# Optimization experiments

Measured on AMD Instinct MI355X. Metric: run time of the kernel, lower is better.

## Reference

```python
import jax, jax.numpy as jnp
import numpy as np

OUTPUT_SIZES = [1, 3, 6, 8]  # SPP pyramid -> total KV length 110

def _bounds(n, out):
    # PyTorch AdaptiveMaxPool2d bin boundaries
    return [((i * n) // out, -((-(i + 1) * n) // out)) for i in range(out)]

def adaptive_max_pool2d(x, out):
    # x: [B, C, H, W] -> [B, C, out, out]
    B, C, H, W = x.shape
    rows = jnp.stack([x[:, :, s:e, :].max(axis=2) for s, e in _bounds(H, out)], axis=2)
    return jnp.stack([rows[:, :, :, s:e].max(axis=3) for s, e in _bounds(W, out)], axis=3)

def spp(x):
    # [B, C, H, W] -> [B, C, S] with S = sum(o*o) = 110
    B, C = x.shape[:2]
    return jnp.concatenate(
        [adaptive_max_pool2d(x, o).reshape(B, C, o * o) for o in OUTPUT_SIZES], axis=2)

def conv1x1(x, w):
    # 1x1 conv, no bias: w [O, C], x [B, C, H, W]
    return jnp.einsum('oc,bchw->bohw', w, x)

def setup_inputs() -> dict:
    key = jax.random.key(0)
    ks = jax.random.split(key, 6)
    B, C, H, W = 16, 512, 64, 64
    IC = C // 2
    x = jax.random.normal(ks[0], (B, C, H, W), jnp.float32)
    y = jax.random.normal(ks[1], (B, C, H, W), jnp.float32)
    sc = 1.0 / np.sqrt(C)
    w_phi = jax.random.normal(ks[2], (IC, C), jnp.float32) * sc
    w_theta = jax.random.normal(ks[3], (IC, C), jnp.float32) * sc
    w_g = jax.random.normal(ks[4], (IC, C), jnp.float32) * sc
    w_mask = jax.random.normal(ks[5], (C, IC), jnp.float32) * (1.0 / np.sqrt(IC))
    return {"x": x, "y": y, "w_phi": w_phi, "w_theta": w_theta,
            "w_g": w_g, "w_mask": w_mask}

def reference(x, y, w_phi, w_theta, w_g, w_mask):
    B, C, H, W = x.shape
    IC = w_phi.shape[0]
    N = H * W
    # Query: [B, N, IC]
    x_phi = conv1x1(x, w_phi).reshape(B, IC, N).transpose(0, 2, 1)
    # Keys/values from SPP-pooled y: [B, IC, S] / [B, S, IC]
    y_theta = spp(conv1x1(y, w_theta))
    y_g = spp(conv1x1(y, w_g)).transpose(0, 2, 1)
    # Attention with softmax over the QUERY axis (dim=1), as in the source
    attn = jax.nn.softmax(jnp.einsum('bnc,bcs->bns', x_phi, y_theta), axis=1)
    agg = jnp.einsum('bns,bsc->bnc', attn, y_g)          # [B, N, IC]
    agg = agg.transpose(0, 2, 1).reshape(B, IC, H, W)     # [B, IC, H, W]
    mask = conv1x1(agg, w_mask)                           # [B, C, H, W]
    return mask + x
```

## Files before the change

### kernel.cpp

```cpp
#include <hip/hip_runtime.h>

#define DI __device__ __forceinline__

typedef __attribute__((ext_vector_type(8))) __bf16 bf16x8;
typedef __attribute__((ext_vector_type(4))) float f32x4;

DI unsigned short f2bf(float x) {
  union { float f; unsigned u; } v; v.f = x;
  unsigned r = v.u + 0x7fffu + ((v.u >> 16) & 1u);
  return (unsigned short)(r >> 16);
}
DI float bf2f(unsigned short h) {
  union { unsigned u; float f; } v; v.u = ((unsigned)h) << 16;
  return v.f;
}
DI unsigned pack2(float a, float b) {
  return (unsigned)f2bf(a) | (((unsigned)f2bf(b)) << 16);
}

__global__ __launch_bounds__(256) void k1_conv_tg(
    const float* __restrict__ y, const float* __restrict__ w_theta,
    const float* __restrict__ w_g, unsigned short* __restrict__ tg)
{
  const int tid = threadIdx.x;
  const int nb = blockIdx.x * 128;
  const int mb = blockIdx.y * 128;
  const int b  = blockIdx.z;
  const int lane = tid & 63, wv = tid >> 6;
  const int wm = (wv & 1) * 64, wn = (wv >> 1) * 64;
  const int l15 = lane & 15, l4 = lane >> 4;

  __shared__ unsigned short Ah[128 * 40];
  __shared__ unsigned short Bt[128 * 40];

  f32x4 acc[4][4];
  #pragma unroll
  for (int i = 0; i < 4; ++i)
    #pragma unroll
    for (int j = 0; j < 4; ++j) acc[i][j] = f32x4{0.f, 0.f, 0.f, 0.f};

  for (int kb = 0; kb < 512; kb += 32) {
    #pragma unroll
    for (int j = 0; j < 4; ++j) {
      int flat = tid + 256 * j;
      int row = flat >> 3, c4 = (flat & 7) << 2;
      int og = mb + row;
      const float* wr = (og < 256) ? (w_theta + (size_t)og * 512)
                                   : (w_g + (size_t)(og - 256) * 512);
      float4 v = *(const float4*)(wr + kb + c4);
      uint2 u; u.x = pack2(v.x, v.y); u.y = pack2(v.z, v.w);
      *(uint2*)&Ah[row * 40 + c4] = u;
    }
    #pragma unroll
    for (int j = 0; j < 2; ++j) {
      int q = tid + 256 * j;
      int cp = q >> 5, n4 = (q & 31) << 2;
      const float* yr = y + ((size_t)(b * 512 + kb) + cp * 2) * 4096 + nb + n4;
      float4 r0 = *(const float4*)yr;
      float4 r1 = *(const float4*)(yr + 4096);
      const float* p0 = (const float*)&r0;
      const float* p1 = (const float*)&r1;
      #pragma unroll
      for (int i = 0; i < 4; ++i)
        *(unsigned*)&Bt[(n4 + i) * 40 + cp * 2] = pack2(p0[i], p1[i]);
    }
    __syncthreads();
    bf16x8 af[4], bfr[4];
    #pragma unroll
    for (int i = 0; i < 4; ++i)
      af[i] = *(const bf16x8*)&Ah[(wm + i * 16 + l15) * 40 + l4 * 8];
    #pragma unroll
    for (int j = 0; j < 4; ++j)
      bfr[j] = *(const bf16x8*)&Bt[(wn + j * 16 + l15) * 40 + l4 * 8];
    #pragma unroll
    for (int i = 0; i < 4; ++i)
      #pragma unroll
      for (int j = 0; j < 4; ++j)
        acc[i][j] = __builtin_amdgcn_mfma_f32_16x16x32_bf16(af[i], bfr[j], acc[i][j], 0, 0, 0);
    __syncthreads();
  }

  #pragma unroll
  for (int i = 0; i < 4; ++i)
    #pragma unroll
    for (int j = 0; j < 4; ++j)
      #pragma unroll
      for (int r = 0; r < 4; ++r) {
        int o = mb + wm + i * 16 + l4 * 4 + r;
        int n = nb + wn + j * 16 + l15;
        tg[((size_t)(b * 512) + o) * 4096 + n] = f2bf(acc[i][j][r]);
      }
}

__constant__ int c_RS[18] = {0, 0,21,42, 0,10,21,32,42,53, 0,8,16,24,32,40,48,56};
__constant__ int c_RE[18] = {64, 22,43,64, 11,22,32,43,54,64, 8,16,24,32,40,48,56,64};

__global__ __launch_bounds__(256) void k2_spp(
    const unsigned short* __restrict__ tg, float* __restrict__ Pt,
    float* __restrict__ Pg)
{
  const int o = blockIdx.x, b = blockIdx.y, tid = threadIdx.x;
  __shared__ float L[64 * 68];
  __shared__ float R[18 * 68];
  const unsigned short* p = tg + ((size_t)(b * 512) + o) * 4096;
  #pragma unroll
  for (int j = 0; j < 2; ++j) {
    int base = tid * 16 + j * 8;
    uint4 u = *(const uint4*)(p + base);
    int h = base >> 6, w = base & 63;
    float* d = &L[h * 68 + w];
    d[0] = bf2f((unsigned short)(u.x & 0xffff)); d[1] = bf2f((unsigned short)(u.x >> 16));
    d[2] = bf2f((unsigned short)(u.y & 0xffff)); d[3] = bf2f((unsigned short)(u.y >> 16));
    d[4] = bf2f((unsigned short)(u.z & 0xffff)); d[5] = bf2f((unsigned short)(u.z >> 16));
    d[6] = bf2f((unsigned short)(u.w & 0xffff)); d[7] = bf2f((unsigned short)(u.w >> 16));
  }
  __syncthreads();
  for (int t = tid; t < 18 * 64; t += 256) {
    int rb = t >> 6, w = t & 63;
    float m = -3.4e38f;
    int e = c_RE[rb];
    for (int h = c_RS[rb]; h < e; ++h) m = fmaxf(m, L[h * 68 + w]);
    R[rb * 68 + w] = m;
  }
  __syncthreads();
  if (tid < 128) {
    float val = 0.f;
    if (tid < 110) {
      int t = tid, rb, cb;
      if (t == 0)      { rb = 0; cb = 0; }
      else if (t < 10) { int i = t - 1;  rb = 1 + i / 3;  cb = 1 + i % 3; }
      else if (t < 46) { int i = t - 10; rb = 4 + i / 6;  cb = 4 + i % 6; }
      else             { int i = t - 46; rb = 10 + i / 8; cb = 10 + i % 8; }
      float m = -3.4e38f;
      int e = c_RE[cb];
      for (int w = c_RS[cb]; w < e; ++w) m = fmaxf(m, R[rb * 68 + w]);
      val = m;
    }
    float* outp = (o < 256) ? Pt : Pg;
    int ch = (o < 256) ? o : (o - 256);
    outp[((size_t)(b * 128) + tid) * 256 + ch] = val;
  }
}

__global__ __launch_bounds__(256) void k3_kmat(
    const float* __restrict__ Pt, const float* __restrict__ w_phi,
    unsigned short* __restrict__ Kth, unsigned short* __restrict__ Ktl)
{
  const int ct = blockIdx.x, b = blockIdx.y, tid = threadIdx.x;
  const int tx = tid & 15, ty = tid >> 4;
  const int c0 = tx * 4, s0 = ty * 8;
  __shared__ float Ls[128 * 64];
  __shared__ float Ws[64 * 68];
  float acc[8][4] = {};
  for (int kc = 0; kc < 256; kc += 64) {
    #pragma unroll
    for (int j = 0; j < 8; ++j) {
      int flat = tid + 256 * j;
      int row = flat >> 4, k4 = (flat & 15) << 2;
      *(float4*)&Ls[row * 64 + k4] =
          *(const float4*)(Pt + ((size_t)(b * 128) + row) * 256 + kc + k4);
    }
    #pragma unroll
    for (int j = 0; j < 4; ++j) {
      int flat = tid + 256 * j;
      int row = flat >> 4, c4 = (flat & 15) << 2;
      *(float4*)&Ws[row * 68 + c4] =
          *(const float4*)(w_phi + (size_t)(kc + row) * 512 + ct * 64 + c4);
    }
    __syncthreads();
    for (int k = 0; k < 64; k += 4) {
      float4 wv[4];
      #pragma unroll
      for (int kk = 0; kk < 4; ++kk) wv[kk] = *(const float4*)&Ws[(k + kk) * 68 + c0];
      #pragma unroll
      for (int i = 0; i < 8; ++i) {
        float4 a = *(const float4*)&Ls[(s0 + i) * 64 + k];
        const float* ap = (const float*)&a;
        #pragma unroll
        for (int kk = 0; kk < 4; ++kk) {
          const float* wp = (const float*)&wv[kk];
          acc[i][0] += ap[kk] * wp[0];
          acc[i][1] += ap[kk] * wp[1];
          acc[i][2] += ap[kk] * wp[2];
          acc[i][3] += ap[kk] * wp[3];
        }
      }
    }
    __syncthreads();
  }
  #pragma unroll
  for (int i = 0; i < 8; ++i) {
    unsigned short hi[4]; float lo[4];
    #pragma unroll
    for (int j = 0; j < 4; ++j) { hi[j] = f2bf(acc[i][j]); lo[j] = acc[i][j] - bf2f(hi[j]); }
    size_t base = ((size_t)(b * 128) + s0 + i) * 512 + ct * 64 + c0;
    uint2 uh; uh.x = (unsigned)hi[0] | ((unsigned)hi[1] << 16);
    uh.y = (unsigned)hi[2] | ((unsigned)hi[3] << 16);
    uint2 ul; ul.x = pack2(lo[0], lo[1]); ul.y = pack2(lo[2], lo[3]);
    *(uint2*)&Kth[base] = uh;
    *(uint2*)&Ktl[base] = ul;
  }
}

__global__ __launch_bounds__(256) void k3_vmat(
    const float* __restrict__ Pg, const float* __restrict__ w_mask,
    float* __restrict__ V)
{
  const int ot = blockIdx.x, b = blockIdx.y, tid = threadIdx.x;
  const int tx = tid & 15, ty = tid >> 4;
  const int o0 = ty * 4;
  __shared__ float Ws[64 * 64];
  __shared__ float Ps[128 * 68];
  float acc[4][8] = {};
  for (int kc = 0; kc < 256; kc += 64) {
    #pragma unroll
    for (int j = 0; j < 4; ++j) {
      int flat = tid + 256 * j;
      int row = flat >> 4, k4 = (flat & 15) << 2;
      *(float4*)&Ws[row * 64 + k4] =
          *(const float4*)(w_mask + (size_t)(ot * 64 + row) * 256 + kc + k4);
    }
    #pragma unroll
    for (int j = 0; j < 8; ++j) {
      int flat = tid + 256 * j;
      int row = flat >> 4, k4 = (flat & 15) << 2;
      *(float4*)&Ps[row * 68 + k4] =
          *(const float4*)(Pg + ((size_t)(b * 128) + row) * 256 + kc + k4);
    }
    __syncthreads();
    for (int k = 0; k < 64; k += 4) {
      float4 wv[4];
      #pragma unroll
      for (int i = 0; i < 4; ++i) wv[i] = *(const float4*)&Ws[(o0 + i) * 64 + k];
      #pragma unroll
      for (int jj = 0; jj < 8; ++jj) {
        float4 pv = *(const float4*)&Ps[(tx + 16 * jj) * 68 + k];
        const float* pp = (const float*)&pv;
        #pragma unroll
        for (int i = 0; i < 4; ++i) {
          const float* wp = (const float*)&wv[i];
          #pragma unroll
          for (int kk = 0; kk < 4; ++kk) acc[i][jj] += wp[kk] * pp[kk];
        }
      }
    }
    __syncthreads();
  }
  #pragma unroll
  for (int i = 0; i < 4; ++i)
    #pragma unroll
    for (int jj = 0; jj < 8; ++jj)
      V[((size_t)(b * 512) + ot * 64 + o0 + i) * 128 + tx + 16 * jj] = acc[i][jj];
}

__global__ __launch_bounds__(256) void k4_scores(
    const float* __restrict__ x, const unsigned short* __restrict__ Kth,
    const unsigned short* __restrict__ Ktl, float* __restrict__ scores)
{
  const int tid = threadIdx.x;
  const int nb = blockIdx.x * 128;
  const int b = blockIdx.y;
  const int lane = tid & 63, wv = tid >> 6;
  const int wm = (wv & 1) * 64, wn = (wv >> 1) * 64;
  const int l15 = lane & 15, l4 = lane >> 4;
  __shared__ unsigned short Ah[128 * 40], Al[128 * 40];
  __shared__ unsigned short Bh[128 * 40], Bl[128 * 40];
  f32x4 acc[4][4];
  #pragma unroll
  for (int i = 0; i < 4; ++i)
    #pragma unroll
    for (int j = 0; j < 4; ++j) acc[i][j] = f32x4{0.f, 0.f, 0.f, 0.f};

  for (int kb = 0; kb < 512; kb += 32) {
    #pragma unroll
    for (int j = 0; j < 4; ++j) {
      int flat = tid + 256 * j;
      int row = flat >> 3, c4 = (flat & 7) << 2;
      size_t g = ((size_t)(b * 128) + row) * 512 + kb + c4;
      *(uint2*)&Ah[row * 40 + c4] = *(const uint2*)(Kth + g);
      *(uint2*)&Al[row * 40 + c4] = *(const uint2*)(Ktl + g);
    }
    #pragma unroll
    for (int j = 0; j < 2; ++j) {
      int q = tid + 256 * j;
      int cp = q >> 5, n4 = (q & 31) << 2;
      const float* xr = x + ((size_t)(b * 512 + kb) + cp * 2) * 4096 + nb + n4;
      float4 r0 = *(const float4*)xr;
      float4 r1 = *(const float4*)(xr + 4096);
      const float* p0 = (const float*)&r0;
      const float* p1 = (const float*)&r1;
      #pragma unroll
      for (int i = 0; i < 4; ++i) {
        unsigned short h0 = f2bf(p0[i]), h1 = f2bf(p1[i]);
        *(unsigned*)&Bh[(n4 + i) * 40 + cp * 2] = (unsigned)h0 | ((unsigned)h1 << 16);
        *(unsigned*)&Bl[(n4 + i) * 40 + cp * 2] = pack2(p0[i] - bf2f(h0), p1[i] - bf2f(h1));
      }
    }
    __syncthreads();
    bf16x8 ah[4], al[4], bh[4], bl[4];
    #pragma unroll
    for (int i = 0; i < 4; ++i) {
      ah[i] = *(const bf16x8*)&Ah[(wm + i * 16 + l15) * 40 + l4 * 8];
      al[i] = *(const bf16x8*)&Al[(wm + i * 16 + l15) * 40 + l4 * 8];
    }
    #pragma unroll
    for (int j = 0; j < 4; ++j) {
      bh[j] = *(const bf16x8*)&Bh[(wn + j * 16 + l15) * 40 + l4 * 8];
      bl[j] = *(const bf16x8*)&Bl[(wn + j * 16 + l15) * 40 + l4 * 8];
    }
    #pragma unroll
    for (int i = 0; i < 4; ++i)
      #pragma unroll
      for (int j = 0; j < 4; ++j) {
        acc[i][j] = __builtin_amdgcn_mfma_f32_16x16x32_bf16(ah[i], bh[j], acc[i][j], 0, 0, 0);
        acc[i][j] = __builtin_amdgcn_mfma_f32_16x16x32_bf16(ah[i], bl[j], acc[i][j], 0, 0, 0);
        acc[i][j] = __builtin_amdgcn_mfma_f32_16x16x32_bf16(al[i], bh[j], acc[i][j], 0, 0, 0);
      }
    __syncthreads();
  }
  #pragma unroll
  for (int i = 0; i < 4; ++i)
    #pragma unroll
    for (int j = 0; j < 4; ++j)
      #pragma unroll
      for (int r = 0; r < 4; ++r)
        scores[((size_t)(b * 128) + wm + i * 16 + l4 * 4 + r) * 4096 + nb + wn + j * 16 + l15] =
            acc[i][j][r];
}

__global__ __launch_bounds__(256) void k5_stats(
    const float* __restrict__ scores, float* __restrict__ mbuf,
    float* __restrict__ lbuf)
{
  const int s = blockIdx.x, b = blockIdx.y, tid = threadIdx.x;
  if (s >= 110) {
    if (tid == 0) { mbuf[b * 128 + s] = 0.f; lbuf[b * 128 + s] = 0.f; }
    return;
  }
  const float* row = scores + ((size_t)(b * 128) + s) * 4096;
  float4 v[4];
  float m = -3.4e38f;
  #pragma unroll
  for (int j = 0; j < 4; ++j) {
    v[j] = *(const float4*)(row + (tid + 256 * j) * 4);
    m = fmaxf(m, fmaxf(fmaxf(v[j].x, v[j].y), fmaxf(v[j].z, v[j].w)));
  }
  #pragma unroll
  for (int off = 32; off > 0; off >>= 1) m = fmaxf(m, __shfl_down(m, off));
  __shared__ float red[8];
  if ((tid & 63) == 0) red[tid >> 6] = m;
  __syncthreads();
  float mm = fmaxf(fmaxf(red[0], red[1]), fmaxf(red[2], red[3]));
  float sum = 0.f;
  #pragma unroll
  for (int j = 0; j < 4; ++j)
    sum += __expf(v[j].x - mm) + __expf(v[j].y - mm) +
           __expf(v[j].z - mm) + __expf(v[j].w - mm);
  #pragma unroll
  for (int off = 32; off > 0; off >>= 1) sum += __shfl_down(sum, off);
  if ((tid & 63) == 0) red[4 + (tid >> 6)] = sum;
  __syncthreads();
  if (tid == 0) {
    float S = red[4] + red[5] + red[6] + red[7];
    mbuf[b * 128 + s] = mm;
    lbuf[b * 128 + s] = 1.f / S;
  }
}

__global__ __launch_bounds__(256) void k5e_expT(
    const float* __restrict__ scores, const float* __restrict__ mbuf,
    unsigned short* __restrict__ Eb)
{
  const int nt = blockIdx.x, b = blockIdx.y, tid = threadIdx.x;
  __shared__ float L[128 * 68];
  __shared__ float sm[128];
  if (tid < 128) sm[tid] = mbuf[b * 128 + tid];
  #pragma unroll
  for (int j = 0; j < 8; ++j) {
    int flat = tid + 256 * j;
    int s = flat >> 4, n4 = (flat & 15) << 2;
    *(float4*)&L[s * 68 + n4] =
        *(const float4*)(scores + ((size_t)(b * 128) + s) * 4096 + nt * 64 + n4);
  }
  __syncthreads();
  int n = tid >> 2, sq = (tid & 3) * 32;
  unsigned ub[16];
  #pragma unroll
  for (int k = 0; k < 32; k += 2) {
    float e0 = __expf(L[(sq + k) * 68 + n] - sm[sq + k]);
    float e1 = __expf(L[(sq + k + 1) * 68 + n] - sm[sq + k + 1]);
    ub[k >> 1] = pack2(e0, e1);
  }
  uint4* dst = (uint4*)(Eb + ((size_t)(b * 4096) + nt * 64 + n) * 128 + sq);
  #pragma unroll
  for (int j = 0; j < 4; ++j)
    dst[j] = make_uint4(ub[4 * j], ub[4 * j + 1], ub[4 * j + 2], ub[4 * j + 3]);
}

__global__ __launch_bounds__(256) void k6_out(
    const unsigned short* __restrict__ Eb, const float* __restrict__ V,
    const float* __restrict__ lbuf, const float* __restrict__ x,
    float* __restrict__ out)
{
  const int tid = threadIdx.x;
  const int nb = blockIdx.x * 128;
  const int mb = blockIdx.y * 128;
  const int b = blockIdx.z;
  const int lane = tid & 63, wv = tid >> 6;
  const int wm = (wv & 1) * 64, wn = (wv >> 1) * 64;
  const int l15 = lane & 15, l4 = lane >> 4;
  __shared__ unsigned short Ah[128 * 72];
  __shared__ unsigned short Bt[128 * 72];
  __shared__ float sl[128];
  if (tid < 128) sl[tid] = lbuf[b * 128 + tid];

  f32x4 acc[4][4];
  #pragma unroll
  for (int i = 0; i < 4; ++i)
    #pragma unroll
    for (int j = 0; j < 4; ++j) acc[i][j] = f32x4{0.f, 0.f, 0.f, 0.f};

  for (int kc = 0; kc < 128; kc += 64) {
    __syncthreads();
    #pragma unroll
    for (int j = 0; j < 8; ++j) {
      int flat = tid + 256 * j;
      int row = flat >> 4, s4 = (flat & 15) << 2;
      float4 v = *(const float4*)(V + ((size_t)(b * 512) + mb + row) * 128 + kc + s4);
      v.x *= sl[kc + s4]; v.y *= sl[kc + s4 + 1];
      v.z *= sl[kc + s4 + 2]; v.w *= sl[kc + s4 + 3];
      uint2 u; u.x = pack2(v.x, v.y); u.y = pack2(v.z, v.w);
      *(uint2*)&Ah[row * 72 + s4] = u;
    }
    #pragma unroll
    for (int j = 0; j < 4; ++j) {
      int flat = tid + 256 * j;
      int n = flat >> 3, s8 = (flat & 7) << 3;
      uint4 u = *(const uint4*)(Eb + ((size_t)(b * 4096) + nb + n) * 128 + kc + s8);
      *(uint4*)&Bt[n * 72 + s8] = u;
    }
    __syncthreads();
    #pragma unroll
    for (int kb = 0; kb < 64; kb += 32) {
      bf16x8 af[4], bfr[4];
      #pragma unroll
      for (int i = 0; i < 4; ++i)
        af[i] = *(const bf16x8*)&Ah[(wm + i * 16 + l15) * 72 + kb + l4 * 8];
      #pragma unroll
      for (int j = 0; j < 4; ++j)
        bfr[j] = *(const bf16x8*)&Bt[(wn + j * 16 + l15) * 72 + kb + l4 * 8];
      #pragma unroll
      for (int i = 0; i < 4; ++i)
        #pragma unroll
        for (int j = 0; j < 4; ++j)
          acc[i][j] = __builtin_amdgcn_mfma_f32_16x16x32_bf16(af[i], bfr[j], acc[i][j], 0, 0, 0);
    }
  }
  #pragma unroll
  for (int i = 0; i < 4; ++i)
    #pragma unroll
    for (int j = 0; j < 4; ++j)
      #pragma unroll
      for (int r = 0; r < 4; ++r) {
        int o = mb + wm + i * 16 + l4 * 4 + r;
        size_t idx = ((size_t)(b * 512) + o) * 4096 + nb + wn + j * 16 + l15;
        out[idx] = acc[i][j][r] + x[idx];
      }
}

extern "C" void kernel_launch(void* const* d_in, const int* in_sizes, int n_in,
                              void* d_out, int out_size, void* d_ws, size_t ws_size,
                              hipStream_t stream)
{
  (void)in_sizes; (void)n_in; (void)out_size; (void)ws_size;
  const float* x       = (const float*)d_in[0];
  const float* y       = (const float*)d_in[1];
  const float* w_phi   = (const float*)d_in[2];
  const float* w_theta = (const float*)d_in[3];
  const float* w_g     = (const float*)d_in[4];
  const float* w_mask  = (const float*)d_in[5];
  float* out = (float*)d_out;

  char* ws = (char*)d_ws;
  unsigned short* tg  = (unsigned short*)ws; ws += 67108864;
  float* scores       = (float*)ws;          ws += 33554432;
  float* Pt           = (float*)ws;          ws += 2097152;
  float* Pg           = (float*)ws;          ws += 2097152;
  unsigned short* Kth = (unsigned short*)ws; ws += 2097152;
  unsigned short* Ktl = (unsigned short*)ws; ws += 2097152;
  float* V            = (float*)ws;          ws += 4194304;
  float* mbuf         = (float*)ws;          ws += 8192;
  float* lbuf         = (float*)ws;          ws += 8192;
  unsigned short* Eb  = (unsigned short*)ws; ws += 16777216;

  k1_conv_tg<<<dim3(32, 4, 16), 256, 0, stream>>>(y, w_theta, w_g, tg);
  k2_spp<<<dim3(512, 16), 256, 0, stream>>>(tg, Pt, Pg);
  k3_kmat<<<dim3(8, 16), 256, 0, stream>>>(Pt, w_phi, Kth, Ktl);
  k3_vmat<<<dim3(8, 16), 256, 0, stream>>>(Pg, w_mask, V);
  k4_scores<<<dim3(32, 16), 256, 0, stream>>>(x, Kth, Ktl, scores);
  k5_stats<<<dim3(128, 16), 256, 0, stream>>>(scores, mbuf, lbuf);
  k5e_expT<<<dim3(64, 16), 256, 0, stream>>>(scores, mbuf, Eb);
  k6_out<<<dim3(32, 4, 16), 256, 0, stream>>>(Eb, V, lbuf, x, out);
}
```

Before: 588.5 us.

## Fuse conv with row pooling, pre-transpose inputs to bf16, drop x split-precision

```diff
diff --git a/kernel.cpp b/kernel.cpp
--- a/kernel.cpp
+++ b/kernel.cpp
@@ -18,20 +18,49 @@
   return (unsigned)f2bf(a) | (((unsigned)f2bf(b)) << 16);
 }
 
-__global__ __launch_bounds__(256) void k1_conv_tg(
-    const float* __restrict__ y, const float* __restrict__ w_theta,
-    const float* __restrict__ w_g, unsigned short* __restrict__ tg)
-{
+__global__ __launch_bounds__(256) void p0_transpose(
+    const float* __restrict__ src, unsigned short* __restrict__ dst)
+{
+  const int n0 = blockIdx.x * 64, c0 = blockIdx.y * 64, b = blockIdx.z;
   const int tid = threadIdx.x;
-  const int nb = blockIdx.x * 128;
-  const int mb = blockIdx.y * 128;
+  __shared__ float T[64 * 65];
+  #pragma unroll
+  for (int p = 0; p < 4; ++p) {
+    int r = p * 16 + (tid >> 4);
+    int n4 = (tid & 15) << 2;
+    *(float4*)&T[r * 65 + n4] =
+        *(const float4*)(src + ((size_t)(b * 512 + c0 + r)) * 4096 + n0 + n4);
+  }
+  __syncthreads();
+  int n = tid >> 2, cc = (tid & 3) * 16;
+  unsigned u[8];
+  #pragma unroll
+  for (int j = 0; j < 16; j += 2)
+    u[j >> 1] = pack2(T[(cc + j) * 65 + n], T[(cc + j + 1) * 65 + n]);
+  unsigned short* d = dst + ((size_t)(b * 4096 + n0 + n)) * 512 + c0 + cc;
+  *(uint4*)(d) = make_uint4(u[0], u[1], u[2], u[3]);
+  *(uint4*)(d + 8) = make_uint4(u[4], u[5], u[6], u[7]);
+}
+
+__constant__ int c_RS[18] = {0, 0,21,42, 0,10,21,32,42,53, 0,8,16,24,32,40,48,56};
+__constant__ int c_RE[18] = {64, 22,43,64, 11,22,32,43,54,64, 8,16,24,32,40,48,56,64};
+
+__global__ __launch_bounds__(256) void k1f_conv_pool(
+    const unsigned short* __restrict__ yT, const float* __restrict__ w_theta,
+    const float* __restrict__ w_g, unsigned short* __restrict__ Rbuf)
+{
+  const int tid = threadIdx.x;
+  const int mb = blockIdx.x * 128;
+  const int nb = blockIdx.y * 128;
   const int b  = blockIdx.z;
   const int lane = tid & 63, wv = tid >> 6;
   const int wm = (wv & 1) * 64, wn = (wv >> 1) * 64;
   const int l15 = lane & 15, l4 = lane >> 4;
 
-  __shared__ unsigned short Ah[128 * 40];
-  __shared__ unsigned short Bt[128 * 40];
+  __shared__ __align__(16) char smem[33280];
+  unsigned short* As = (unsigned short*)smem;
+  unsigned short* Bs = (unsigned short*)(smem + 10240);
+  float* P = (float*)smem;
 
   f32x4 acc[4][4];
   #pragma unroll
@@ -49,29 +78,23 @@
                                    : (w_g + (size_t)(og - 256) * 512);
       float4 v = *(const float4*)(wr + kb + c4);
       uint2 u; u.x = pack2(v.x, v.y); u.y = pack2(v.z, v.w);
-      *(uint2*)&Ah[row * 40 + c4] = u;
-    }
-    #pragma unroll
-    for (int j = 0; j < 2; ++j) {
-      int q = tid + 256 * j;
-      int cp = q >> 5, n4 = (q & 31) << 2;
-      const float* yr = y + ((size_t)(b * 512 + kb) + cp * 2) * 4096 + nb + n4;
-      float4 r0 = *(const float4*)yr;
-      float4 r1 = *(const float4*)(yr + 4096);
-      const float* p0 = (const float*)&r0;
-      const float* p1 = (const float*)&r1;
-      #pragma unroll
-      for (int i = 0; i < 4; ++i)
-        *(unsigned*)&Bt[(n4 + i) * 40 + cp * 2] = pack2(p0[i], p1[i]);
+      *(uint2*)&As[row * 40 + c4] = u;
+    }
+    #pragma unroll
+    for (int p = 0; p < 2; ++p) {
+      int q = tid + 256 * p;
+      int row = q >> 2, s8 = (q & 3) << 3;
+      *(uint4*)&Bs[row * 40 + s8] =
+          *(const uint4*)(yT + ((size_t)(b * 4096 + nb + row)) * 512 + kb + s8);
     }
     __syncthreads();
     bf16x8 af[4], bfr[4];
     #pragma unroll
     for (int i = 0; i < 4; ++i)
-      af[i] = *(const bf16x8*)&Ah[(wm + i * 16 + l15) * 40 + l4 * 8];
+      af[i] = *(const bf16x8*)&As[(wm + i * 16 + l15) * 40 + l4 * 8];
     #pragma unroll
     for (int j = 0; j < 4; ++j)
-      bfr[j] = *(const bf16x8*)&Bt[(wn + j * 16 + l15) * 40 + l4 * 8];
+      bfr[j] = *(const bf16x8*)&Bs[(wn + j * 16 + l15) * 40 + l4 * 8];
     #pragma unroll
     for (int i = 0; i < 4; ++i)
       #pragma unroll
@@ -80,66 +103,81 @@
     __syncthreads();
   }
 
-  #pragma unroll
-  for (int i = 0; i < 4; ++i)
-    #pragma unroll
-    for (int j = 0; j < 4; ++j)
-      #pragma unroll
-      for (int r = 0; r < 4; ++r) {
-        int o = mb + wm + i * 16 + l4 * 4 + r;
-        int n = nb + wn + j * 16 + l15;
-        tg[((size_t)(b * 512) + o) * 4096 + n] = f2bf(acc[i][j][r]);
+  const int hloc = wv >> 1;
+  #pragma unroll
+  for (int pass = 0; pass < 2; ++pass) {
+    __syncthreads();
+    if (hloc == pass) {
+      #pragma unroll
+      for (int i = 0; i < 4; ++i)
+        #pragma unroll
+        for (int j = 0; j < 4; ++j)
+          #pragma unroll
+          for (int r = 0; r < 4; ++r)
+            P[(wm + i * 16 + l4 * 4 + r) * 65 + j * 16 + l15] = acc[i][j][r];
+    }
+    __syncthreads();
+    const int o = tid & 127;
+    size_t rbase = (((size_t)(b * 64 + blockIdx.y * 2 + pass)) * 18) * 512 + mb + o;
+    if (tid < 128) {
+      float b0 = -3.4e38f, b1 = b0, b2 = b0, b3 = b0;
+      #pragma unroll
+      for (int w = 0; w < 64; ++w) {
+        float v = P[o * 65 + w];
+        b0 = fmaxf(b0, v);
+        if (w < 22) b1 = fmaxf(b1, v);
+        if (w >= 21 && w < 43) b2 = fmaxf(b2, v);
+        if (w >= 42) b3 = fmaxf(b3, v);
       }
-}
-
-__constant__ int c_RS[18] = {0, 0,21,42, 0,10,21,32,42,53, 0,8,16,24,32,40,48,56};
-__constant__ int c_RE[18] = {64, 22,43,64, 11,22,32,43,54,64, 8,16,24,32,40,48,56,64};
-
-__global__ __launch_bounds__(256) void k2_spp(
-    const unsigned short* __restrict__ tg, float* __restrict__ Pt,
+      Rbuf[rbase]           = f2bf(b0);
+      Rbuf[rbase + 512]     = f2bf(b1);
+      Rbuf[rbase + 2 * 512] = f2bf(b2);
+      Rbuf[rbase + 3 * 512] = f2bf(b3);
+    } else {
+      float s6[6], s8[8];
+      #pragma unroll
+      for (int i = 0; i < 6; ++i) s6[i] = -3.4e38f;
+      #pragma unroll
+      for (int i = 0; i < 8; ++i) s8[i] = -3.4e38f;
+      constexpr int R6S[6] = {0, 10, 21, 32, 42, 53};
+      constexpr int R6E[6] = {11, 22, 32, 43, 54, 64};
+      #pragma unroll
+      for (int w = 0; w < 64; ++w) {
+        float v = P[o * 65 + w];
+        #pragma unroll
+        for (int i = 0; i < 6; ++i)
+          if (w >= R6S[i] && w < R6E[i]) s6[i] = fmaxf(s6[i], v);
+        s8[w >> 3] = fmaxf(s8[w >> 3], v);
+      }
+      #pragma unroll
+      for (int i = 0; i < 6; ++i) Rbuf[rbase + (size_t)(4 + i) * 512] = f2bf(s6[i]);
+      #pragma unroll
+      for (int i = 0; i < 8; ++i) Rbuf[rbase + (size_t)(10 + i) * 512] = f2bf(s8[i]);
+    }
+  }
+}
+
+__global__ __launch_bounds__(256) void k2_pool_final(
+    const unsigned short* __restrict__ Rbuf, float* __restrict__ Pt,
     float* __restrict__ Pg)
 {
-  const int o = blockIdx.x, b = blockIdx.y, tid = threadIdx.x;
-  __shared__ float L[64 * 68];
-  __shared__ float R[18 * 68];
-  const unsigned short* p = tg + ((size_t)(b * 512) + o) * 4096;
-  #pragma unroll
-  for (int j = 0; j < 2; ++j) {
-    int base = tid * 16 + j * 8;
-    uint4 u = *(const uint4*)(p + base);
-    int h = base >> 6, w = base & 63;
-    float* d = &L[h * 68 + w];
-    d[0] = bf2f((unsigned short)(u.x & 0xffff)); d[1] = bf2f((unsigned short)(u.x >> 16));
-    d[2] = bf2f((unsigned short)(u.y & 0xffff)); d[3] = bf2f((unsigned short)(u.y >> 16));
-    d[4] = bf2f((unsigned short)(u.z & 0xffff)); d[5] = bf2f((unsigned short)(u.z >> 16));
-    d[6] = bf2f((unsigned short)(u.w & 0xffff)); d[7] = bf2f((unsigned short)(u.w >> 16));
-  }
-  __syncthreads();
-  for (int t = tid; t < 18 * 64; t += 256) {
-    int rb = t >> 6, w = t & 63;
-    float m = -3.4e38f;
-    int e = c_RE[rb];
-    for (int h = c_RS[rb]; h < e; ++h) m = fmaxf(m, L[h * 68 + w]);
-    R[rb * 68 + w] = m;
-  }
-  __syncthreads();
-  if (tid < 128) {
-    float val = 0.f;
-    if (tid < 110) {
-      int t = tid, rb, cb;
-      if (t == 0)      { rb = 0; cb = 0; }
-      else if (t < 10) { int i = t - 1;  rb = 1 + i / 3;  cb = 1 + i % 3; }
-      else if (t < 46) { int i = t - 10; rb = 4 + i / 6;  cb = 4 + i % 6; }
-      else             { int i = t - 46; rb = 10 + i / 8; cb = 10 + i % 8; }
-      float m = -3.4e38f;
-      int e = c_RE[cb];
-      for (int w = c_RS[cb]; w < e; ++w) m = fmaxf(m, R[rb * 68 + w]);
-      val = m;
-    }
-    float* outp = (o < 256) ? Pt : Pg;
-    int ch = (o < 256) ? o : (o - 256);
-    outp[((size_t)(b * 128) + tid) * 256 + ch] = val;
-  }
+  const int s = blockIdx.x, b = blockIdx.y, tid = threadIdx.x;
+  size_t obase = ((size_t)(b * 128) + s) * 256 + tid;
+  if (s >= 110) { Pt[obase] = 0.f; Pg[obase] = 0.f; return; }
+  int he, wb;
+  if (s == 0)      { he = 0; wb = 0; }
+  else if (s < 10) { int i = s - 1;  he = 1 + i / 3;  wb = 1 + i % 3; }
+  else if (s < 46) { int i = s - 10; he = 4 + i / 6;  wb = 4 + i % 6; }
+  else             { int i = s - 46; he = 10 + i / 8; wb = 10 + i % 8; }
+  float m0 = -3.4e38f, m1 = -3.4e38f;
+  int e = c_RE[he];
+  for (int h = c_RS[he]; h < e; ++h) {
+    const unsigned short* r = Rbuf + (((size_t)(b * 64 + h)) * 18 + wb) * 512;
+    m0 = fmaxf(m0, bf2f(r[tid]));
+    m1 = fmaxf(m1, bf2f(r[tid + 256]));
+  }
+  Pt[obase] = m0;
+  Pg[obase] = m1;
 }
 
 __global__ __launch_bounds__(256) void k3_kmat(
@@ -254,7 +292,7 @@
 }
 
 __global__ __launch_bounds__(256) void k4_scores(
-    const float* __restrict__ x, const unsigned short* __restrict__ Kth,
+    const unsigned short* __restrict__ xT, const unsigned short* __restrict__ Kth,
     const unsigned short* __restrict__ Ktl, float* __restrict__ scores)
 {
   const int tid = threadIdx.x;
@@ -263,8 +301,7 @@
   const int lane = tid & 63, wv = tid >> 6;
   const int wm = (wv & 1) * 64, wn = (wv >> 1) * 64;
   const int l15 = lane & 15, l4 = lane >> 4;
-  __shared__ unsigned short Ah[128 * 40], Al[128 * 40];
-  __shared__ unsigned short Bh[128 * 40], Bl[128 * 40];
+  __shared__ unsigned short Ah[128 * 40], Al[128 * 40], Bs[128 * 40];
   f32x4 acc[4][4];
   #pragma unroll
   for (int i = 0; i < 4; ++i)
@@ -273,48 +310,36 @@
 
   for (int kb = 0; kb < 512; kb += 32) {
     #pragma unroll
-    for (int j = 0; j < 4; ++j) {
-      int flat = tid + 256 * j;
-      int row = flat >> 3, c4 = (flat & 7) << 2;
-      size_t g = ((size_t)(b * 128) + row) * 512 + kb + c4;
-      *(uint2*)&Ah[row * 40 + c4] = *(const uint2*)(Kth + g);
-      *(uint2*)&Al[row * 40 + c4] = *(const uint2*)(Ktl + g);
-    }
-    #pragma unroll
-    for (int j = 0; j < 2; ++j) {
-      int q = tid + 256 * j;
-      int cp = q >> 5, n4 = (q & 31) << 2;
-      const float* xr = x + ((size_t)(b * 512 + kb) + cp * 2) * 4096 + nb + n4;
-      float4 r0 = *(const float4*)xr;
-      float4 r1 = *(const float4*)(xr + 4096);
-      const float* p0 = (const float*)&r0;
-      const float* p1 = (const float*)&r1;
-      #pragma unroll
-      for (int i = 0; i < 4; ++i) {
-        unsigned short h0 = f2bf(p0[i]), h1 = f2bf(p1[i]);
-        *(unsigned*)&Bh[(n4 + i) * 40 + cp * 2] = (unsigned)h0 | ((unsigned)h1 << 16);
-        *(unsigned*)&Bl[(n4 + i) * 40 + cp * 2] = pack2(p0[i] - bf2f(h0), p1[i] - bf2f(h1));
-      }
-    }
-    __syncthreads();
-    bf16x8 ah[4], al[4], bh[4], bl[4];
+    for (int p = 0; p < 2; ++p) {
+      int q = tid + 256 * p;
+      int row = q >> 2, s8 = (q & 3) << 3;
+      size_t g = ((size_t)(b * 128) + row) * 512 + kb + s8;
+      *(uint4*)&Ah[row * 40 + s8] = *(const uint4*)(Kth + g);
+      *(uint4*)&Al[row * 40 + s8] = *(const uint4*)(Ktl + g);
+    }
+    #pragma unroll
+    for (int p = 0; p < 2; ++p) {
+      int q = tid + 256 * p;
+      int row = q >> 2, s8 = (q & 3) << 3;
+      *(uint4*)&Bs[row * 40 + s8] =
+          *(const uint4*)(xT + ((size_t)(b * 4096 + nb + row)) * 512 + kb + s8);
+    }
+    __syncthreads();
+    bf16x8 ah[4], al[4], bfr[4];
     #pragma unroll
     for (int i = 0; i < 4; ++i) {
       ah[i] = *(const bf16x8*)&Ah[(wm + i * 16 + l15) * 40 + l4 * 8];
       al[i] = *(const bf16x8*)&Al[(wm + i * 16 + l15) * 40 + l4 * 8];
     }
     #pragma unroll
-    for (int j = 0; j < 4; ++j) {
-      bh[j] = *(const bf16x8*)&Bh[(wn + j * 16 + l15) * 40 + l4 * 8];
-      bl[j] = *(const bf16x8*)&Bl[(wn + j * 16 + l15) * 40 + l4 * 8];
-    }
+    for (int j = 0; j < 4; ++j)
+      bfr[j] = *(const bf16x8*)&Bs[(wn + j * 16 + l15) * 40 + l4 * 8];
     #pragma unroll
     for (int i = 0; i < 4; ++i)
       #pragma unroll
       for (int j = 0; j < 4; ++j) {
-        acc[i][j] = __builtin_amdgcn_mfma_f32_16x16x32_bf16(ah[i], bh[j], acc[i][j], 0, 0, 0);
-        acc[i][j] = __builtin_amdgcn_mfma_f32_16x16x32_bf16(ah[i], bl[j], acc[i][j], 0, 0, 0);
-        acc[i][j] = __builtin_amdgcn_mfma_f32_16x16x32_bf16(al[i], bh[j], acc[i][j], 0, 0, 0);
+        acc[i][j] = __builtin_amdgcn_mfma_f32_16x16x32_bf16(ah[i], bfr[j], acc[i][j], 0, 0, 0);
+        acc[i][j] = __builtin_amdgcn_mfma_f32_16x16x32_bf16(al[i], bfr[j], acc[i][j], 0, 0, 0);
       }
     __syncthreads();
   }
@@ -436,8 +461,8 @@
     for (int j = 0; j < 4; ++j) {
       int flat = tid + 256 * j;
       int n = flat >> 3, s8 = (flat & 7) << 3;
-      uint4 u = *(const uint4*)(Eb + ((size_t)(b * 4096) + nb + n) * 128 + kc + s8);
-      *(uint4*)&Bt[n * 72 + s8] = u;
+      *(uint4*)&Bt[n * 72 + s8] =
+          *(const uint4*)(Eb + ((size_t)(b * 4096) + nb + n) * 128 + kc + s8);
     }
     __syncthreads();
     #pragma unroll
@@ -482,22 +507,28 @@
   float* out = (float*)d_out;
 
   char* ws = (char*)d_ws;
-  unsigned short* tg  = (unsigned short*)ws; ws += 67108864;
-  float* scores       = (float*)ws;          ws += 33554432;
-  float* Pt           = (float*)ws;          ws += 2097152;
-  float* Pg           = (float*)ws;          ws += 2097152;
-  unsigned short* Kth = (unsigned short*)ws; ws += 2097152;
-  unsigned short* Ktl = (unsigned short*)ws; ws += 2097152;
-  float* V            = (float*)ws;          ws += 4194304;
-  float* mbuf         = (float*)ws;          ws += 8192;
-  float* lbuf         = (float*)ws;          ws += 8192;
-  unsigned short* Eb  = (unsigned short*)ws; ws += 16777216;
-
-  k1_conv_tg<<<dim3(32, 4, 16), 256, 0, stream>>>(y, w_theta, w_g, tg);
-  k2_spp<<<dim3(512, 16), 256, 0, stream>>>(tg, Pt, Pg);
+  unsigned short* yT = (unsigned short*)ws;
+  unsigned short* xT = yT;
+  char* B0 = ws + 67108864;
+  unsigned short* Rbuf = (unsigned short*)B0;
+  float* scores = (float*)B0;
+  unsigned short* Eb = (unsigned short*)(B0 + 33554432);
+  float* V = (float*)(B0 + 50331648);
+  char* C0 = B0 + 54525952;
+  float* Pt = (float*)C0;
+  float* Pg = (float*)(C0 + 2097152);
+  unsigned short* Kth = (unsigned short*)(C0 + 4194304);
+  unsigned short* Ktl = (unsigned short*)(C0 + 6291456);
+  float* mbuf = (float*)(C0 + 8388608);
+  float* lbuf = (float*)(C0 + 8396800);
+
+  p0_transpose<<<dim3(64, 8, 16), 256, 0, stream>>>(y, yT);
+  k1f_conv_pool<<<dim3(4, 32, 16), 256, 0, stream>>>(yT, w_theta, w_g, Rbuf);
+  k2_pool_final<<<dim3(128, 16), 256, 0, stream>>>(Rbuf, Pt, Pg);
   k3_kmat<<<dim3(8, 16), 256, 0, stream>>>(Pt, w_phi, Kth, Ktl);
   k3_vmat<<<dim3(8, 16), 256, 0, stream>>>(Pg, w_mask, V);
-  k4_scores<<<dim3(32, 16), 256, 0, stream>>>(x, Kth, Ktl, scores);
+  p0_transpose<<<dim3(64, 8, 16), 256, 0, stream>>>(x, xT);
+  k4_scores<<<dim3(32, 16), 256, 0, stream>>>(xT, Kth, Ktl, scores);
   k5_stats<<<dim3(128, 16), 256, 0, stream>>>(scores, mbuf, lbuf);
   k5e_expT<<<dim3(64, 16), 256, 0, stream>>>(scores, mbuf, Eb);
   k6_out<<<dim3(32, 4, 16), 256, 0, stream>>>(Eb, V, lbuf, x, out);
```

New measurement: 561.4 us. -4.6%, faster.
